# Kernel tuning notes

Measured on AMD Instinct MI355X. Metric: run time of the kernel, lower is better.

The kernel has to match this reference:

```python
import jax, jax.numpy as jnp
import numpy as np

MARGIN = 1.0
RULE_WEIGHT = 0.5
NUM_ENT = 100000
NUM_REL = 500
DIM = 512
N_RULES = 20


def setup_inputs() -> dict:
    key = jax.random.key(0)
    ks = jax.random.split(key, 8)
    pos_triples = jax.random.randint(ks[0], (1024, 3), 0, NUM_REL)
    neg_triples = jax.random.randint(ks[1], (8192, 3), 0, NUM_REL)
    rule_r1 = jax.random.randint(ks[2], (N_RULES,), 0, NUM_REL)
    rule_r2 = jax.random.randint(ks[3], (N_RULES,), 0, NUM_REL)
    rule_conf = jax.random.uniform(ks[4], (N_RULES,), dtype=jnp.float32)
    ent_emb = jax.random.normal(ks[5], (NUM_ENT, DIM), dtype=jnp.float32)
    rel_emb = jax.random.normal(ks[6], (NUM_REL, DIM), dtype=jnp.float32)
    norm_vec = jax.random.normal(ks[7], (NUM_REL, DIM), dtype=jnp.float32)
    return {
        "pos_triples": pos_triples, "neg_triples": neg_triples,
        "rule_r1": rule_r1, "rule_r2": rule_r2, "rule_conf": rule_conf,
        "ent_emb": ent_emb, "rel_emb": rel_emb, "norm_vec": norm_vec,
    }


def _transh_dist(h_idx, r_idx, t_idx, ent_emb, rel_emb, norm_vec):
    """TransH distance ||proj(h) + r - proj(t)||_2.
    Index args may have any broadcast-compatible shape; returns that shape."""
    w = norm_vec[r_idx]                                   # [..., d]
    w = w / jnp.linalg.norm(w, axis=-1, keepdims=True)
    he = ent_emb[h_idx]
    te = ent_emb[t_idx]
    re = rel_emb[r_idx]
    hp = he - jnp.sum(he * w, axis=-1, keepdims=True) * w  # hyperplane projection
    tp = te - jnp.sum(te * w, axis=-1, keepdims=True) * w
    return jnp.linalg.norm(hp + re - tp, axis=-1)


def reference(pos_triples, neg_triples, rule_r1, rule_r2, rule_conf,
              ent_emb, rel_emb, norm_vec):
    B = pos_triples.shape[0]
    neg_ratio = neg_triples.shape[0] // B
    # basic margin ranking loss: pos triples repeat-interleaved to align with negs
    exp_pos = jnp.repeat(pos_triples, neg_ratio, axis=0)   # [B*ratio, 3]
    d_pos = _transh_dist(exp_pos[:, 0], exp_pos[:, 1], exp_pos[:, 2],
                         ent_emb, rel_emb, norm_vec)
    d_neg = _transh_dist(neg_triples[:, 0], neg_triples[:, 1], neg_triples[:, 2],
                         ent_emb, rel_emb, norm_vec)
    basic_loss = jnp.mean(jax.nn.relu(MARGIN + d_pos - d_neg))

    # rule loss: for each pos triple i and rule j with r_i == r1_j,
    # rule_loss -= conf_j * score(h_i, r2_j, t_i), score = -distance.
    h = pos_triples[:, 0][:, None]        # [B,1]
    r = pos_triples[:, 1][:, None]        # [B,1]
    t = pos_triples[:, 2][:, None]        # [B,1]
    d_rule = _transh_dist(h, rule_r2[None, :], t, ent_emb, rel_emb, norm_vec)  # [B,nR]
    score = -d_rule
    mask = (r == rule_r1[None, :]).astype(score.dtype)     # [B,nR]
    rule_loss = -jnp.sum(mask * rule_conf[None, :] * score)

    return basic_loss + RULE_WEIGHT * rule_loss
```

## Files before the change

### kernel.cpp

```cpp
#include <hip/hip_runtime.h>

#define DIM        512
#define B_POS      1024
#define N_NEG      8192
#define N_RULES    20
#define NEG_RATIO  8
#define NBLK       2048

__device__ __forceinline__ float wave_sum(float x) {
#pragma unroll
    for (int off = 32; off > 0; off >>= 1)
        x += __shfl_xor(x, off, 64);
    return x;
}

__device__ __forceinline__ float transh_dist(
    int h, int r, int t,
    const float* __restrict__ ent, const float* __restrict__ rel,
    const float* __restrict__ nv, int lane)
{
    const float4* wp = (const float4*)(nv  + (size_t)r * DIM);
    const float4* hp = (const float4*)(ent + (size_t)h * DIM);
    const float4* tp = (const float4*)(ent + (size_t)t * DIM);
    const float4* rp = (const float4*)(rel + (size_t)r * DIM);

    float4 wv[2], dv[2], rv[2];
    float ww = 0.f, dw = 0.f;
#pragma unroll
    for (int c = 0; c < 2; ++c) {
        float4 w  = wp[lane + 64 * c];
        float4 hh = hp[lane + 64 * c];
        float4 tt = tp[lane + 64 * c];
        float4 rr = rp[lane + 64 * c];
        float4 d;
        d.x = hh.x - tt.x; d.y = hh.y - tt.y; d.z = hh.z - tt.z; d.w = hh.w - tt.w;
        wv[c] = w; dv[c] = d; rv[c] = rr;
        ww += w.x * w.x + w.y * w.y + w.z * w.z + w.w * w.w;
        dw += d.x * w.x + d.y * w.y + d.z * w.z + d.w * w.w;
    }
    ww = wave_sum(ww);
    dw = wave_sum(dw);
    float s = dw / ww;

    float ss = 0.f;
#pragma unroll
    for (int c = 0; c < 2; ++c) {
        float vx = dv[c].x + rv[c].x - s * wv[c].x;
        float vy = dv[c].y + rv[c].y - s * wv[c].y;
        float vz = dv[c].z + rv[c].z - s * wv[c].z;
        float vw = dv[c].w + rv[c].w - s * wv[c].w;
        ss += vx * vx + vy * vy + vz * vz + vw * vw;
    }
    ss = wave_sum(ss);
    return sqrtf(ss);
}

__global__ __launch_bounds__(256) void fused_kernel(
    const int* __restrict__ pos, const int* __restrict__ neg,
    const int* __restrict__ rule_r1, const int* __restrict__ rule_r2,
    const float* __restrict__ rule_conf,
    const float* __restrict__ ent, const float* __restrict__ rel,
    const float* __restrict__ nv,
    float* __restrict__ partial)
{
    int w    = threadIdx.x >> 6;
    int lane = threadIdx.x & 63;
    int n    = blockIdx.x * 4 + w;
    int i    = n >> 3;
    int k    = n & 7;

    int h = pos[3 * i], r = pos[3 * i + 1], t = pos[3 * i + 2];
    float dp = transh_dist(h, r, t, ent, rel, nv, lane);
    float dn = transh_dist(neg[3 * n], neg[3 * n + 1], neg[3 * n + 2],
                           ent, rel, nv, lane);
    float v = 1.0f + dp - dn;
    float contrib = ((v > 0.f) ? v : 0.f) * (1.0f / (float)N_NEG);

    float racc = 0.f;
#pragma unroll
    for (int m = 0; m < 3; ++m) {
        int j = k + 8 * m;
        if (j < N_RULES && r == rule_r1[j]) {
            float d = transh_dist(h, rule_r2[j], t, ent, rel, nv, lane);
            racc += rule_conf[j] * d;
        }
    }
    contrib += 0.5f * racc;

    __shared__ float part[4];
    if (lane == 0) part[w] = contrib;
    __syncthreads();
    if (threadIdx.x == 0)
        partial[blockIdx.x] = part[0] + part[1] + part[2] + part[3];
}

__global__ __launch_bounds__(256) void final_reduce(
    const float* __restrict__ partial, float* __restrict__ out)
{
    int t = threadIdx.x;
    float s = 0.f;
#pragma unroll
    for (int m = 0; m < NBLK / 256; ++m)
        s += partial[t + 256 * m];
    s = wave_sum(s);
    __shared__ float part[4];
    int w = t >> 6, lane = t & 63;
    if (lane == 0) part[w] = s;
    __syncthreads();
    if (t == 0) out[0] = part[0] + part[1] + part[2] + part[3];
}

extern "C" void kernel_launch(void* const* d_in, const int* in_sizes, int n_in,
                              void* d_out, int out_size, void* d_ws, size_t ws_size,
                              hipStream_t stream) {
    const int*   pos       = (const int*)  d_in[0];
    const int*   neg       = (const int*)  d_in[1];
    const int*   rule_r1   = (const int*)  d_in[2];
    const int*   rule_r2   = (const int*)  d_in[3];
    const float* rule_conf = (const float*)d_in[4];
    const float* ent       = (const float*)d_in[5];
    const float* rel       = (const float*)d_in[6];
    const float* nv        = (const float*)d_in[7];
    float* out     = (float*)d_out;
    float* partial = (float*)d_ws;

    fused_kernel<<<NBLK, 256, 0, stream>>>(pos, neg, rule_r1, rule_r2, rule_conf,
                                           ent, rel, nv, partial);
    final_reduce<<<1, 256, 0, stream>>>(partial, out);
}
```

Before: 252.5 us.

## Precompute positive distances once and expand TransH distance algebraically

Splits the fused kernel into a positive/rule kernel, which computes each positive distance once, and a negative kernel that reads the stored positive distance. The old kernel recomputed each positive distance eight times. The distance is rewritten in closed form from four dot products reduced in a single interleaved shuffle pass, replacing the previous two dependent reductions. Rule distances reuse the loaded h-t difference across rules. This adds a kernel launch and a dependency between kernels, and the expanded formula can lose precision through cancellation, which is clamped at zero.

```diff
diff --git a/kernel.cpp b/kernel.cpp
--- a/kernel.cpp
+++ b/kernel.cpp
@@ -4,8 +4,19 @@
 #define B_POS      1024
 #define N_NEG      8192
 #define N_RULES    20
-#define NEG_RATIO  8
-#define NBLK       2048
+#define NBLK_NEG   2048
+#define NBLK_POS   256
+#define NPART      (NBLK_NEG + NBLK_POS)
+
+__device__ __forceinline__ float4 f4sub(float4 a, float4 b) {
+    return make_float4(a.x - b.x, a.y - b.y, a.z - b.z, a.w - b.w);
+}
+__device__ __forceinline__ float4 f4add(float4 a, float4 b) {
+    return make_float4(a.x + b.x, a.y + b.y, a.z + b.z, a.w + b.w);
+}
+__device__ __forceinline__ float dot4(float4 a, float4 b) {
+    return a.x * b.x + a.y * b.y + a.z * b.z + a.w * b.w;
+}
 
 __device__ __forceinline__ float wave_sum(float x) {
 #pragma unroll
@@ -14,78 +25,79 @@
     return x;
 }
 
-__device__ __forceinline__ float transh_dist(
-    int h, int r, int t,
-    const float* __restrict__ ent, const float* __restrict__ rel,
-    const float* __restrict__ nv, int lane)
+__device__ __forceinline__ float dist_from_d(
+    float4 d0, float4 d1, int r,
+    const float* __restrict__ rel, const float* __restrict__ nv, int lane)
 {
     const float4* wp = (const float4*)(nv  + (size_t)r * DIM);
-    const float4* hp = (const float4*)(ent + (size_t)h * DIM);
-    const float4* tp = (const float4*)(ent + (size_t)t * DIM);
     const float4* rp = (const float4*)(rel + (size_t)r * DIM);
-
-    float4 wv[2], dv[2], rv[2];
-    float ww = 0.f, dw = 0.f;
+    float4 w0 = wp[lane], w1 = wp[lane + 64];
+    float4 r0 = rp[lane], r1 = rp[lane + 64];
+    float4 s0 = f4add(d0, r0), s1 = f4add(d1, r1);
+    float a  = dot4(s0, s0) + dot4(s1, s1);
+    float b  = dot4(d0, w0) + dot4(d1, w1);
+    float ww = dot4(w0, w0) + dot4(w1, w1);
+    float rw = dot4(r0, w0) + dot4(r1, w1);
 #pragma unroll
-    for (int c = 0; c < 2; ++c) {
-        float4 w  = wp[lane + 64 * c];
-        float4 hh = hp[lane + 64 * c];
-        float4 tt = tp[lane + 64 * c];
-        float4 rr = rp[lane + 64 * c];
-        float4 d;
-        d.x = hh.x - tt.x; d.y = hh.y - tt.y; d.z = hh.z - tt.z; d.w = hh.w - tt.w;
-        wv[c] = w; dv[c] = d; rv[c] = rr;
-        ww += w.x * w.x + w.y * w.y + w.z * w.z + w.w * w.w;
-        dw += d.x * w.x + d.y * w.y + d.z * w.z + d.w * w.w;
+    for (int off = 32; off > 0; off >>= 1) {
+        a  += __shfl_xor(a,  off, 64);
+        b  += __shfl_xor(b,  off, 64);
+        ww += __shfl_xor(ww, off, 64);
+        rw += __shfl_xor(rw, off, 64);
     }
-    ww = wave_sum(ww);
-    dw = wave_sum(dw);
-    float s = dw / ww;
-
-    float ss = 0.f;
-#pragma unroll
-    for (int c = 0; c < 2; ++c) {
-        float vx = dv[c].x + rv[c].x - s * wv[c].x;
-        float vy = dv[c].y + rv[c].y - s * wv[c].y;
-        float vz = dv[c].z + rv[c].z - s * wv[c].z;
-        float vw = dv[c].w + rv[c].w - s * wv[c].w;
-        ss += vx * vx + vy * vy + vz * vz + vw * vw;
-    }
-    ss = wave_sum(ss);
-    return sqrtf(ss);
+    return sqrtf(fmaxf(a - b * (b + 2.f * rw) / ww, 0.f));
 }
 
-__global__ __launch_bounds__(256) void fused_kernel(
-    const int* __restrict__ pos, const int* __restrict__ neg,
+__global__ __launch_bounds__(256) void pos_rule_kernel(
+    const int* __restrict__ pos,
     const int* __restrict__ rule_r1, const int* __restrict__ rule_r2,
     const float* __restrict__ rule_conf,
     const float* __restrict__ ent, const float* __restrict__ rel,
     const float* __restrict__ nv,
+    float* __restrict__ d_pos, float* __restrict__ rulepart)
+{
+    int w = threadIdx.x >> 6, lane = threadIdx.x & 63;
+    int i = blockIdx.x * 4 + w;
+    int h = pos[3 * i], r = pos[3 * i + 1], t = pos[3 * i + 2];
+    const float4* hp = (const float4*)(ent + (size_t)h * DIM);
+    const float4* tp = (const float4*)(ent + (size_t)t * DIM);
+    float4 d0 = f4sub(hp[lane],      tp[lane]);
+    float4 d1 = f4sub(hp[lane + 64], tp[lane + 64]);
+
+    float dp = dist_from_d(d0, d1, r, rel, nv, lane);
+    if (lane == 0) d_pos[i] = dp;
+
+    float racc = 0.f;
+#pragma unroll 1
+    for (int j = 0; j < N_RULES; ++j) {
+        if (r == rule_r1[j]) {
+            racc += rule_conf[j] * dist_from_d(d0, d1, rule_r2[j], rel, nv, lane);
+        }
+    }
+    __shared__ float part[4];
+    if (lane == 0) part[w] = 0.5f * racc;
+    __syncthreads();
+    if (threadIdx.x == 0)
+        rulepart[blockIdx.x] = part[0] + part[1] + part[2] + part[3];
+}
+
+__global__ __launch_bounds__(256) void neg_kernel(
+    const int* __restrict__ neg, const float* __restrict__ d_pos,
+    const float* __restrict__ ent, const float* __restrict__ rel,
+    const float* __restrict__ nv,
     float* __restrict__ partial)
 {
-    int w    = threadIdx.x >> 6;
-    int lane = threadIdx.x & 63;
-    int n    = blockIdx.x * 4 + w;
-    int i    = n >> 3;
-    int k    = n & 7;
+    int w = threadIdx.x >> 6, lane = threadIdx.x & 63;
+    int n = blockIdx.x * 4 + w;
+    int h = neg[3 * n], r = neg[3 * n + 1], t = neg[3 * n + 2];
+    const float4* hp = (const float4*)(ent + (size_t)h * DIM);
+    const float4* tp = (const float4*)(ent + (size_t)t * DIM);
+    float4 d0 = f4sub(hp[lane],      tp[lane]);
+    float4 d1 = f4sub(hp[lane + 64], tp[lane + 64]);
 
-    int h = pos[3 * i], r = pos[3 * i + 1], t = pos[3 * i + 2];
-    float dp = transh_dist(h, r, t, ent, rel, nv, lane);
-    float dn = transh_dist(neg[3 * n], neg[3 * n + 1], neg[3 * n + 2],
-                           ent, rel, nv, lane);
-    float v = 1.0f + dp - dn;
+    float dn = dist_from_d(d0, d1, r, rel, nv, lane);
+    float v = 1.0f + d_pos[n >> 3] - dn;
     float contrib = ((v > 0.f) ? v : 0.f) * (1.0f / (float)N_NEG);
-
-    float racc = 0.f;
-#pragma unroll
-    for (int m = 0; m < 3; ++m) {
-        int j = k + 8 * m;
-        if (j < N_RULES && r == rule_r1[j]) {
-            float d = transh_dist(h, rule_r2[j], t, ent, rel, nv, lane);
-            racc += rule_conf[j] * d;
-        }
-    }
-    contrib += 0.5f * racc;
 
     __shared__ float part[4];
     if (lane == 0) part[w] = contrib;
@@ -100,7 +112,7 @@
     int t = threadIdx.x;
     float s = 0.f;
 #pragma unroll
-    for (int m = 0; m < NBLK / 256; ++m)
+    for (int m = 0; m < NPART / 256; ++m)
         s += partial[t + 256 * m];
     s = wave_sum(s);
     __shared__ float part[4];
@@ -121,10 +133,14 @@
     const float* ent       = (const float*)d_in[5];
     const float* rel       = (const float*)d_in[6];
     const float* nv        = (const float*)d_in[7];
-    float* out     = (float*)d_out;
-    float* partial = (float*)d_ws;
+    float* out = (float*)d_out;
 
-    fused_kernel<<<NBLK, 256, 0, stream>>>(pos, neg, rule_r1, rule_r2, rule_conf,
-                                           ent, rel, nv, partial);
+    float* partial  = (float*)d_ws;
+    float* rulepart = partial + NBLK_NEG;
+    float* d_pos    = partial + NPART;
+
+    pos_rule_kernel<<<NBLK_POS, 256, 0, stream>>>(pos, rule_r1, rule_r2, rule_conf,
+                                                  ent, rel, nv, d_pos, rulepart);
+    neg_kernel<<<NBLK_NEG, 256, 0, stream>>>(neg, d_pos, ent, rel, nv, partial);
     final_reduce<<<1, 256, 0, stream>>>(partial, out);
 }
```

Measured after the change: 252.6 us. Within noise of the previous version (+0.0%).
